# Performance work log

Hardware: AMD Instinct MI355X
Metric: run time of the kernel (lower is better)

The kernel has to match this reference:

```python
import jax, jax.numpy as jnp
import numpy as np

N, I, O, G = 16384, 128, 128, 16


def setup_inputs() -> dict:
    key = jax.random.key(0)
    k1, k2, k3 = jax.random.split(key, 3)
    coef_norm = np.sqrt(I) * np.sqrt(G)  # smooth_initialization=False
    return {
        "x": jax.random.normal(k1, (N, I), dtype=jnp.float32),
        "cos_amplitudes": jax.random.normal(k2, (O, I, G), dtype=jnp.float32) / coef_norm,
        "sin_amplitudes": jax.random.normal(k3, (O, I, G), dtype=jnp.float32) / coef_norm,
        "bias": jnp.zeros((O,), dtype=jnp.float32),
        "ln_gamma": jnp.ones((O,), dtype=jnp.float32),
        "ln_beta": jnp.zeros((O,), dtype=jnp.float32),
    }


def reference(x, cos_amplitudes, sin_amplitudes, bias, ln_gamma, ln_beta):
    g = cos_amplitudes.shape[-1]
    # frequencies buffer: init_freq_scale=1.0 -> [1, 2, ..., grid_size]
    freqs = jnp.arange(1, g + 1, dtype=x.dtype)  # (G,)
    phases = x[:, :, None] * freqs               # (N, I, G)
    # contraction expressed as a GEMM instead of broadcast-sum over (N,O,I,G)
    out = jnp.einsum("nig,oig->no", jnp.cos(phases), cos_amplitudes)
    out = out + jnp.einsum("nig,oig->no", jnp.sin(phases), sin_amplitudes)
    out = out + bias  # (N, O)
    # LayerNorm over output_dim, eps=1e-5 (torch default)
    mu = jnp.mean(out, axis=-1, keepdims=True)
    var = jnp.var(out, axis=-1, keepdims=True)
    out = (out - mu) / jnp.sqrt(var + 1e-5) * ln_gamma + ln_beta
    return out
```

## Files before the change

### kernel.cpp

```cpp
#include <hip/hip_runtime.h>
#include <hip/hip_bf16.h>
#include <math.h>

#define N_TOK 16384
#define I_DIM 128
#define O_DIM 128
#define G_DIM 16
#define BN 32
#define CI 4
#define KC (CI * G_DIM * 2)
#define NCHUNK (I_DIM / CI)
#define A_STRIDE 136
#define ABUF (BN * A_STRIDE)
#define C_STRIDE 132
#define PK_STRIDE 68

typedef __bf16 bf16x8 __attribute__((ext_vector_type(8)));
typedef float  f32x4  __attribute__((ext_vector_type(4)));

__global__ __launch_bounds__(256) void fkan_pack_b(
    const float* __restrict__ cosA, const float* __restrict__ sinA,
    __bf16* __restrict__ Bp)
{
    __shared__ __align__(16) float cosL[32 * PK_STRIDE];
    __shared__ __align__(16) float sinL[32 * PK_STRIDE];
    const int b = blockIdx.x;
    const int t = threadIdx.x;
    const int c = b >> 2, cg = b & 3;

    {
        const int o_l = t >> 3;
        const int k   = t & 7;
        const float* srcc = cosA + ((size_t)(cg * 32 + o_l) * I_DIM + c * 4) * G_DIM;
        const float* srcs = sinA + ((size_t)(cg * 32 + o_l) * I_DIM + c * 4) * G_DIM;
#pragma unroll
        for (int h = 0; h < 2; ++h) {
            int col = (k + 8 * h) * 4;
            *(float4*)(cosL + o_l * PK_STRIDE + col) = *(const float4*)(srcc + col);
            *(float4*)(sinL + o_l * PK_STRIDE + col) = *(const float4*)(srcs + col);
        }
    }
    __syncthreads();

#pragma unroll
    for (int h = 0; h < 2; ++h) {
        int gi    = t + 256 * h;
        int fl    = gi >> 6;
        int lane  = gi & 63;
        int ks    = fl >> 1, ot = fl & 1;
        int row16 = lane & 15, quad = lane >> 4;
        int orow  = ot * 16 + row16;
        int colb  = ks * 16 + quad * 4;
        bf16x8 v;
#pragma unroll
        for (int j = 0; j < 4; ++j) {
            v[2 * j]     = (__bf16)cosL[orow * PK_STRIDE + colb + j];
            v[2 * j + 1] = (__bf16)sinL[orow * PK_STRIDE + colb + j];
        }
        *(bf16x8*)(Bp + ((size_t)b * 512 + gi) * 8) = v;
    }
}

__global__ __launch_bounds__(256, 2) void fkan_main(
    const float* __restrict__ x,
    const __bf16* __restrict__ Bp,
    const float* __restrict__ bias,
    const float* __restrict__ gamma,
    const float* __restrict__ beta,
    float* __restrict__ out)
{
    __shared__ __align__(16) __bf16 smem[2 * ABUF];
    __bf16* A0 = smem;
    __bf16* A1 = smem + ABUF;

    const int t     = threadIdx.x;
    const int lane  = t & 63;
    const int cg    = t >> 6;
    const int row16 = lane & 15;
    const int quad  = lane >> 4;
    const int n0    = blockIdx.x * BN;

    const int srow  = (t & 127) >> 2;
    const int sil   = t & 3;
    const int shalf = t >> 7;

    f32x4 acc[2][2];
#pragma unroll
    for (int mt = 0; mt < 2; ++mt)
#pragma unroll
        for (int ot = 0; ot < 2; ++ot)
            acc[mt][ot] = (f32x4){0.f, 0.f, 0.f, 0.f};

    bf16x8 bA[2][4], bB[2][4];

    auto ld_x = [&](int c) -> float {
        return x[(size_t)(n0 + srow) * I_DIM + c * CI + sil];
    };

    auto ld_b = [&](int c, bf16x8 (&b)[2][4]) {
        const bf16x8* base = (const bf16x8*)Bp + ((size_t)(c * 4 + cg) * 8) * 64 + lane;
#pragma unroll
        for (int ks = 0; ks < 4; ++ks)
#pragma unroll
            for (int ot = 0; ot < 2; ++ot)
                b[ot][ks] = base[(ks * 2 + ot) * 64];
    };

    auto stage_a = [&](float xv, __bf16* Ab) {
        float s1, c1;
        __sincosf(xv, &s1, &c1);
        float cb = c1, sb = s1;
        if (shalf) {
            float cd = c1, sd = s1;
#pragma unroll
            for (int d = 0; d < 3; ++d) {
                float cn = cd * cd - sd * sd;
                float sn = 2.f * cd * sd;
                cd = cn; sd = sn;
            }
            cb = cd * c1 - sd * s1;
            sb = sd * c1 + cd * s1;
        }
        __align__(16) __bf16 feat[16];
        float cc_ = cb, ss_ = sb;
#pragma unroll
        for (int j = 0; j < 8; ++j) {
            feat[2 * j]     = (__bf16)cc_;
            feat[2 * j + 1] = (__bf16)ss_;
            float cn = cc_ * c1 - ss_ * s1;
            float sn = ss_ * c1 + cc_ * s1;
            cc_ = cn; ss_ = sn;
        }
        bf16x8* dst = (bf16x8*)(Ab + srow * A_STRIDE + sil * 32 + shalf * 16);
        dst[0] = ((const bf16x8*)feat)[0];
        dst[1] = ((const bf16x8*)feat)[1];
    };

    auto phase = [&](int c, const __bf16* Ar, __bf16* Aw,
                     bf16x8 (&bcur)[2][4], bf16x8 (&bnext)[2][4], float xs, float& xn) {
        const bool pf = (c + 1 < NCHUNK);
        if (pf) ld_b(c + 1, bnext);
        if (c + 2 < NCHUNK) xn = ld_x(c + 2);
        __builtin_amdgcn_sched_barrier(0);
        if (pf) stage_a(xs, Aw);

        __builtin_amdgcn_s_setprio(1);
#pragma unroll
        for (int ks = 0; ks < 4; ++ks) {
            bf16x8 a0 = *(const bf16x8*)(Ar + (row16)      * A_STRIDE + ks * 32 + quad * 8);
            bf16x8 a1 = *(const bf16x8*)(Ar + (16 + row16) * A_STRIDE + ks * 32 + quad * 8);
            acc[0][0] = __builtin_amdgcn_mfma_f32_16x16x32_bf16(a0, bcur[0][ks], acc[0][0], 0, 0, 0);
            acc[0][1] = __builtin_amdgcn_mfma_f32_16x16x32_bf16(a0, bcur[1][ks], acc[0][1], 0, 0, 0);
            acc[1][0] = __builtin_amdgcn_mfma_f32_16x16x32_bf16(a1, bcur[0][ks], acc[1][0], 0, 0, 0);
            acc[1][1] = __builtin_amdgcn_mfma_f32_16x16x32_bf16(a1, bcur[1][ks], acc[1][1], 0, 0, 0);
        }
        __builtin_amdgcn_s_setprio(0);

        asm volatile("s_waitcnt lgkmcnt(0)" ::: "memory");
        __builtin_amdgcn_sched_barrier(0);
        __builtin_amdgcn_s_barrier();
    };

    float xA = ld_x(0);
    float xB;
    ld_b(0, bA);
    stage_a(xA, A0);
    xB = ld_x(1);
    asm volatile("s_waitcnt lgkmcnt(0)" ::: "memory");
    __builtin_amdgcn_s_barrier();

    for (int cc = 0; cc < NCHUNK / 2; ++cc) {
        phase(2 * cc,     A0, A1, bA, bB, xB, xA);
        phase(2 * cc + 1, A1, A0, bB, bA, xA, xB);
    }

    float* Cs = (float*)smem;
#pragma unroll
    for (int mt = 0; mt < 2; ++mt)
#pragma unroll
        for (int ot = 0; ot < 2; ++ot)
#pragma unroll
            for (int r = 0; r < 4; ++r)
                Cs[(mt * 16 + quad * 4 + r) * C_STRIDE
                   + cg * 32 + ot * 16 + row16] = acc[mt][ot][r];
    __syncthreads();

    {
        const int r  = t >> 3;
        const int oc = t & 7;
        const float* crow = Cs + r * C_STRIDE + oc * 16;
        float vals[16];
        float sum = 0.f, sumsq = 0.f;
#pragma unroll
        for (int j4 = 0; j4 < 4; ++j4) {
            f32x4 v4 = *(const f32x4*)(crow + 4 * j4);
#pragma unroll
            for (int e = 0; e < 4; ++e) {
                float v = v4[e] + bias[oc * 16 + 4 * j4 + e];
                vals[4 * j4 + e] = v;
                sum += v;
                sumsq += v * v;
            }
        }
        sum   += __shfl_xor(sum, 1);   sum   += __shfl_xor(sum, 2);   sum   += __shfl_xor(sum, 4);
        sumsq += __shfl_xor(sumsq, 1); sumsq += __shfl_xor(sumsq, 2); sumsq += __shfl_xor(sumsq, 4);
        float mu   = sum * (1.0f / O_DIM);
        float var  = sumsq * (1.0f / O_DIM) - mu * mu;
        float rstd = rsqrtf(var + 1e-5f);

        float* orow = out + (size_t)(n0 + r) * O_DIM + oc * 16;
#pragma unroll
        for (int j4 = 0; j4 < 4; ++j4) {
            float4 o4;
            o4.x = (vals[4*j4+0] - mu) * rstd * gamma[oc*16 + 4*j4+0] + beta[oc*16 + 4*j4+0];
            o4.y = (vals[4*j4+1] - mu) * rstd * gamma[oc*16 + 4*j4+1] + beta[oc*16 + 4*j4+1];
            o4.z = (vals[4*j4+2] - mu) * rstd * gamma[oc*16 + 4*j4+2] + beta[oc*16 + 4*j4+2];
            o4.w = (vals[4*j4+3] - mu) * rstd * gamma[oc*16 + 4*j4+3] + beta[oc*16 + 4*j4+3];
            *(float4*)(orow + 4 * j4) = o4;
        }
    }
}

extern "C" void kernel_launch(void* const* d_in, const int* in_sizes, int n_in,
                              void* d_out, int out_size, void* d_ws, size_t ws_size,
                              hipStream_t stream) {
    const float* x     = (const float*)d_in[0];
    const float* cosA  = (const float*)d_in[1];
    const float* sinA  = (const float*)d_in[2];
    const float* bias  = (const float*)d_in[3];
    const float* gamma = (const float*)d_in[4];
    const float* beta  = (const float*)d_in[5];
    float* out = (float*)d_out;

    __bf16* Bp = (__bf16*)d_ws;

    fkan_pack_b<<<dim3(128), dim3(256), 0, stream>>>(cosA, sinA, Bp);
    fkan_main<<<dim3(N_TOK / BN), dim3(256), 0, stream>>>(x, Bp, bias, gamma, beta, out);
}
```

Before: 101.7 us.

## Double the K chunk per pipeline stage and compute all 16 harmonics per thread

Raises the per-stage input chunk from 4 to 8 input features, so each main-loop iteration runs 8 MFMA k-steps and half as many barriers. Each thread now produces all 16 cos/sin harmonics of one x value by recurrence instead of splitting them across two thread halves. Also removes one sched_barrier so the compiler can interleave the loads with the harmonic computation. In exchange it doubles the B register prefetch (more VGPRs, with occupancy risk under launch_bounds 256,2), doubles LDS per buffer, and lengthens the serial recurrence chain, which may add bf16 error.

New measurement: 98.72 us. 2.9% less time.

```diff
diff --git a/kernel.cpp b/kernel.cpp
--- a/kernel.cpp
+++ b/kernel.cpp
@@ -7,10 +7,11 @@
 #define O_DIM 128
 #define G_DIM 16
 #define BN 32
-#define CI 4
+#define CI 8
 #define KC (CI * G_DIM * 2)
 #define NCHUNK (I_DIM / CI)
-#define A_STRIDE 136
+#define KSTEPS (KC / 32)
+#define A_STRIDE 264
 #define ABUF (BN * A_STRIDE)
 #define C_STRIDE 132
 #define PK_STRIDE 68
@@ -80,9 +81,8 @@
     const int quad  = lane >> 4;
     const int n0    = blockIdx.x * BN;
 
-    const int srow  = (t & 127) >> 2;
-    const int sil   = t & 3;
-    const int shalf = t >> 7;
+    const int srow  = t >> 3;
+    const int sil   = t & 7;
 
     f32x4 acc[2][2];
 #pragma unroll
@@ -91,62 +91,55 @@
         for (int ot = 0; ot < 2; ++ot)
             acc[mt][ot] = (f32x4){0.f, 0.f, 0.f, 0.f};
 
-    bf16x8 bA[2][4], bB[2][4];
+    bf16x8 bA[2][KSTEPS], bB[2][KSTEPS];
 
     auto ld_x = [&](int c) -> float {
         return x[(size_t)(n0 + srow) * I_DIM + c * CI + sil];
     };
 
-    auto ld_b = [&](int c, bf16x8 (&b)[2][4]) {
-        const bf16x8* base = (const bf16x8*)Bp + ((size_t)(c * 4 + cg) * 8) * 64 + lane;
-#pragma unroll
-        for (int ks = 0; ks < 4; ++ks)
-#pragma unroll
-            for (int ot = 0; ot < 2; ++ot)
-                b[ot][ks] = base[(ks * 2 + ot) * 64];
+    auto ld_b = [&](int c, bf16x8 (&b)[2][KSTEPS]) {
+#pragma unroll
+        for (int ks = 0; ks < KSTEPS; ++ks) {
+            int cO = c * 2 + (ks >> 2);
+            const bf16x8* base = (const bf16x8*)Bp
+                + (((size_t)(cO * 4 + cg) * 8) + (size_t)(ks & 3) * 2) * 64 + lane;
+            b[0][ks] = base[0];
+            b[1][ks] = base[64];
+        }
     };
 
     auto stage_a = [&](float xv, __bf16* Ab) {
         float s1, c1;
         __sincosf(xv, &s1, &c1);
-        float cb = c1, sb = s1;
-        if (shalf) {
-            float cd = c1, sd = s1;
-#pragma unroll
-            for (int d = 0; d < 3; ++d) {
-                float cn = cd * cd - sd * sd;
-                float sn = 2.f * cd * sd;
-                cd = cn; sd = sn;
-            }
-            cb = cd * c1 - sd * s1;
-            sb = sd * c1 + cd * s1;
-        }
-        __align__(16) __bf16 feat[16];
-        float cc_ = cb, ss_ = sb;
-#pragma unroll
-        for (int j = 0; j < 8; ++j) {
-            feat[2 * j]     = (__bf16)cc_;
-            feat[2 * j + 1] = (__bf16)ss_;
-            float cn = cc_ * c1 - ss_ * s1;
-            float sn = ss_ * c1 + cc_ * s1;
-            cc_ = cn; ss_ = sn;
-        }
-        bf16x8* dst = (bf16x8*)(Ab + srow * A_STRIDE + sil * 32 + shalf * 16);
-        dst[0] = ((const bf16x8*)feat)[0];
-        dst[1] = ((const bf16x8*)feat)[1];
+        __align__(16) __bf16 feat[32];
+        feat[0] = (__bf16)c1;
+        feat[1] = (__bf16)s1;
+        float ck = c1, sk = s1;
+#pragma unroll
+        for (int g = 1; g < 16; ++g) {
+            float cn = ck * c1 - sk * s1;
+            float sn = sk * c1 + ck * s1;
+            feat[2 * g]     = (__bf16)cn;
+            feat[2 * g + 1] = (__bf16)sn;
+            ck = cn; sk = sn;
+        }
+        bf16x8* dst = (bf16x8*)(Ab + srow * A_STRIDE + sil * 32);
+        const bf16x8* srcv = (const bf16x8*)feat;
+#pragma unroll
+        for (int j = 0; j < 4; ++j) dst[j] = srcv[j];
     };
 
     auto phase = [&](int c, const __bf16* Ar, __bf16* Aw,
-                     bf16x8 (&bcur)[2][4], bf16x8 (&bnext)[2][4], float xs, float& xn) {
+                     bf16x8 (&bcur)[2][KSTEPS], bf16x8 (&bnext)[2][KSTEPS],
+                     float xs, float& xn) {
         const bool pf = (c + 1 < NCHUNK);
         if (pf) ld_b(c + 1, bnext);
         if (c + 2 < NCHUNK) xn = ld_x(c + 2);
-        __builtin_amdgcn_sched_barrier(0);
         if (pf) stage_a(xs, Aw);
 
         __builtin_amdgcn_s_setprio(1);
 #pragma unroll
-        for (int ks = 0; ks < 4; ++ks) {
+        for (int ks = 0; ks < KSTEPS; ++ks) {
             bf16x8 a0 = *(const bf16x8*)(Ar + (row16)      * A_STRIDE + ks * 32 + quad * 8);
             bf16x8 a1 = *(const bf16x8*)(Ar + (16 + row16) * A_STRIDE + ks * 32 + quad * 8);
             acc[0][0] = __builtin_amdgcn_mfma_f32_16x16x32_bf16(a0, bcur[0][ks], acc[0][0], 0, 0, 0);
```
